# Performance work log

Hardware: AMD Instinct MI355X
Metric: run time of the kernel (lower is better)

The kernel has to match this reference:

```python
import jax, jax.numpy as jnp
import numpy as np

B, S, H, N, NREL = 16, 2048, 1024, 128, 8


def setup_inputs() -> dict:
    key = jax.random.key(0)
    ks = jax.random.split(key, 8)
    word_emb = jax.random.normal(ks[0], (B, S, H), dtype=jnp.float32)
    num_ids = jax.random.randint(ks[1], (B, N), 0, S)  # all valid (no -1 padding)
    is_response = jax.random.randint(ks[2], (B, N), 0, 2).astype(jnp.int32)
    numbers = jax.random.normal(ks[3], (B, N), dtype=jnp.float32)
    scale = 1.0 / np.sqrt(H).astype(np.float32)
    w_alpha = jax.random.normal(ks[4], (H, 1), dtype=jnp.float32) * scale
    b_alpha = jnp.zeros((1,), dtype=jnp.float32)
    w_f = jax.random.normal(ks[5], (H, H), dtype=jnp.float32) * scale
    b_f = jnp.zeros((H,), dtype=jnp.float32)
    W_r = jax.random.normal(ks[6], (NREL, H, H), dtype=jnp.float32) * scale  # 8 bias-free relation linears
    return dict(word_emb=word_emb, num_ids=num_ids, is_response=is_response,
                numbers=numbers, w_alpha=w_alpha, b_alpha=b_alpha,
                w_f=w_f, b_f=b_f, W_r=W_r)


def reference(word_emb, num_ids, is_response, numbers, w_alpha, b_alpha, w_f, b_f, W_r):
    Bn, Sn, Hn = word_emb.shape
    Nn = num_ids.shape[1]
    mask = (num_ids >= 0)  # [B,N] valid-node mask (original uses -1 padding)
    idx = jnp.clip(num_ids, 0, Sn - 1)
    # per-batch gather: Init[b,n] = word_emb[b, num_ids[b,n]]  -> [B,N,H]
    Init = jnp.take_along_axis(word_emb, idx[:, :, None], axis=1)
    alpha = jax.nn.sigmoid(Init @ w_alpha + b_alpha)  # [B,N,1]
    # all 8 relation transforms of every sender node j: T[b,r,j,:] = Init[b,j] @ W_r[r].T
    T = jnp.einsum('bnh,rkh->brnk', Init, W_r)  # [B,8,N,H]
    # relation id r(b,i,j) = 4*(num_i>num_j) + 2*resp_i + resp_j
    gt = (numbers[:, :, None] > numbers[:, None, :]).astype(jnp.int32)  # [B,N,N]
    resp = (is_response == 1).astype(jnp.int32)
    R = 4 * gt + 2 * resp[:, :, None] + resp[:, None, :]  # [B,N,N]
    sel = jax.nn.one_hot(R, NREL, dtype=word_emb.dtype)  # [B,N,N,8]
    not_diag = ~jnp.eye(Nn, dtype=bool)
    # edge weight over sender j: alpha_j, valid i & j, i != j
    wgt = (alpha[:, None, :, 0] * mask[:, None, :] * mask[:, :, None]
           * not_diag[None]).astype(word_emb.dtype)  # [B,N,N]
    Temp = jnp.einsum('bijr,brjh->bih', sel * wgt[..., None], T)  # [B,N,H]
    n_nodes = mask.sum(axis=1)  # [B]
    denom = jnp.maximum(n_nodes - 1, 1).astype(word_emb.dtype)
    Temp = Temp / denom[:, None, None]
    out = jax.nn.relu(Init @ w_f + b_f + Temp)  # [B,N,H]
    return out
```

## Files before the change

kernel.cpp:

```cpp
#include <hip/hip_runtime.h>
#include <hip/hip_bf16.h>
#include <stdint.h>

#define B_ 16
#define S_ 2048
#define H_ 1024
#define N_ 128
#define M_ (B_*N_)
#define K5 5120
#define MP 2176

typedef __attribute__((ext_vector_type(8))) short s8vec;
typedef __attribute__((ext_vector_type(4))) short s4vec;
typedef __attribute__((ext_vector_type(4))) float f4vec;
typedef __hip_bfloat16 bf16;

__global__ void k_sortmeta(const int* __restrict__ num_ids, const int* __restrict__ is_resp,
                           const float* __restrict__ numbers,
                           int* __restrict__ sigma, int* __restrict__ newgrp,
                           int* __restrict__ respv, float* __restrict__ denom,
                           int* __restrict__ aperm, int* __restrict__ iperm,
                           int* __restrict__ meta) {
    __shared__ float nums_s[2048];
    __shared__ int sig_s[2048];
    __shared__ int s0[1024], s1[1024];
    __shared__ int cnt_s[16];
    int t = threadIdx.x;
    int g0 = 2*t, g1 = 2*t + 1;
    int b = g0 >> 7;
    int i0 = g0 & 127, i1 = g1 & 127;
    float n0 = numbers[g0], n1 = numbers[g1];
    int id0 = num_ids[g0], id1 = num_ids[g1];
    int v0 = (id0 >= 0) ? 1 : 0, v1 = (id1 >= 0) ? 1 : 0;
    int rsp0 = (is_resp[g0] == 1) ? 1 : 0, rsp1 = (is_resp[g1] == 1) ? 1 : 0;
    nums_s[g0] = n0; nums_s[g1] = n1;
    if (t < 16) cnt_s[t] = 0;
    aperm[t] = -1; aperm[t + 1024] = -1;
    if (t < MP - 2048) aperm[t + 2048] = -1;
    __syncthreads();
    const float* nb = nums_s + b*N_;
    int p0 = 0, p1 = 0;
    for (int j = 0; j < N_; ++j) {
        float nj = nb[j];
        p0 += (nj < n0 || (nj == n0 && j < i0)) ? 1 : 0;
        p1 += (nj < n1 || (nj == n1 && j < i1)) ? 1 : 0;
    }
    sig_s[b*N_ + p0] = i0;
    sig_s[b*N_ + p1] = i1;
    atomicAdd(&cnt_s[b], v0 + v1);
    __syncthreads();
    sigma[g0] = sig_s[g0]; sigma[g1] = sig_s[g1];
    {
        int cur = sig_s[g0];
        int prv = (i0 > 0) ? sig_s[g0-1] : 0;
        newgrp[g0] = (i0 == 0 || nb[cur] != nb[prv]) ? 1 : 0;
        cur = sig_s[g1];
        prv = sig_s[g1-1];
        newgrp[g1] = (nb[cur] != nb[prv]) ? 1 : 0;
    }
    respv[g0] = rsp0 | (v0 << 1);
    respv[g1] = rsp1 | (v1 << 1);
    if (t < 16) denom[t] = fmaxf((float)(cnt_s[t] - 1), 1.0f);
    int a0 = 1 - rsp0, b0 = 1 - rsp1;
    s0[t] = a0 + b0;
    s1[t] = rsp0 + rsp1;
    __syncthreads();
    for (int off = 1; off < 1024; off <<= 1) {
        int w0 = (t >= off) ? s0[t-off] : 0;
        int w1 = (t >= off) ? s1[t-off] : 0;
        __syncthreads();
        s0[t] += w0; s1[t] += w1;
        __syncthreads();
    }
    int C0 = s0[1023], C1 = s1[1023];
    int P0 = ((C0 + 127) >> 7) << 7;
    int ex0 = s0[t] - (a0 + b0);
    int ex1 = s1[t] - (rsp0 + rsp1);
    int p_a = (rsp0 == 0) ? ex0 : P0 + ex1;
    int p_b = (rsp1 == 0) ? ex0 + a0 : P0 + ex1 + rsp0;
    aperm[p_a] = g0; iperm[g0] = p_a;
    aperm[p_b] = g1; iperm[g1] = p_b;
    if (t == 0) { meta[0] = P0; meta[1] = C0; meta[2] = C1; }
}

__global__ void k_prep(const float* __restrict__ word_emb, const int* __restrict__ num_ids,
                       const float* __restrict__ w_alpha, const float* __restrict__ b_alpha,
                       const float* __restrict__ denom, const int* __restrict__ iperm,
                       const float* __restrict__ W_r, const float* __restrict__ w_f,
                       bf16* __restrict__ A, float* __restrict__ ascaled,
                       bf16* __restrict__ Wt) {
    __shared__ float lds[64][65];
    int bid = blockIdx.x;
    int t = threadIdx.x;
    if (bid < 2048) {
        int b = bid >> 7, n = bid & 127;
        int idv = num_ids[b*N_ + n];
        int valid = (idv >= 0) ? 1 : 0;
        int idx = idv < 0 ? 0 : (idv > S_-1 ? S_-1 : idv);
        int pr = iperm[b*N_ + n];
        const float4* row = (const float4*)(word_emb + ((size_t)b*S_ + idx)*H_);
        float4 v = row[t];
        float4 w = ((const float4*)w_alpha)[t];
        float part = v.x*w.x + v.y*w.y + v.z*w.z + v.w*w.w;
        union { s4vec v4; bf16 h[4]; } pk;
        pk.h[0] = __float2bfloat16(v.x);
        pk.h[1] = __float2bfloat16(v.y);
        pk.h[2] = __float2bfloat16(v.z);
        pk.h[3] = __float2bfloat16(v.w);
        *(s4vec*)(A + (size_t)pr*K5 + 4*H_ + t*4) = pk.v4;
#pragma unroll
        for (int off = 32; off > 0; off >>= 1) part += __shfl_down(part, off, 64);
        if ((t & 63) == 0) lds[0][t >> 6] = part;
        __syncthreads();
        if (t == 0) {
            float dot = lds[0][0] + lds[0][1] + lds[0][2] + lds[0][3] + b_alpha[0];
            float al = 1.0f / (1.0f + __expf(-dot));
            ascaled[b*N_ + n] = valid ? (al / denom[b]) : 0.0f;
        }
        return;
    }
    if (bid < 6144) {
        size_t o = ((size_t)(bid - 2048)*256 + t)*8;
        int cs = (int)(o >> 20);
        int c = cs >> 2, s = cs & 3;
        int r = ((s >> 1) << 2) + 2*c + (s & 1);
        size_t off = o & (size_t)(H_*H_ - 1);
        const float4* src = (const float4*)(W_r + (size_t)r*H_*H_ + off);
        float4 v0 = src[0], v1 = src[1];
        union { s8vec v8; bf16 h[8]; } pk;
        pk.h[0] = __float2bfloat16(v0.x); pk.h[1] = __float2bfloat16(v0.y);
        pk.h[2] = __float2bfloat16(v0.z); pk.h[3] = __float2bfloat16(v0.w);
        pk.h[4] = __float2bfloat16(v1.x); pk.h[5] = __float2bfloat16(v1.y);
        pk.h[6] = __float2bfloat16(v1.z); pk.h[7] = __float2bfloat16(v1.w);
        *(s8vec*)(Wt + (size_t)(c*5 + s)*H_*H_ + off) = pk.v8;
        return;
    }
    int bb = bid - 6144;
    int bi = bb & 15, bj = bb >> 4;
    int ty = t >> 4, tx = t & 15;
#pragma unroll
    for (int i = 0; i < 4; ++i) {
        int r = ty*4 + i;
        float4 v = *(const float4*)(w_f + (size_t)(bi*64 + r)*H_ + bj*64 + tx*4);
        lds[r][tx*4+0] = v.x; lds[r][tx*4+1] = v.y;
        lds[r][tx*4+2] = v.z; lds[r][tx*4+3] = v.w;
    }
    __syncthreads();
    bf16* d0 = Wt + (size_t)4*H_*H_;
    bf16* d1 = Wt + (size_t)9*H_*H_;
#pragma unroll
    for (int i = 0; i < 4; ++i) {
        int n = ty*4 + i;
        size_t doff = (size_t)(bj*64 + n)*H_ + bi*64 + tx*4;
        union { s4vec v4; bf16 h[4]; } pk;
#pragma unroll
        for (int j = 0; j < 4; ++j) pk.h[j] = __float2bfloat16(lds[tx*4+j][n]);
        *(s4vec*)(d0 + doff) = pk.v4;
        *(s4vec*)(d1 + doff) = pk.v4;
    }
}

__global__ void k_build(const float* __restrict__ ascaled, const int* __restrict__ sigma,
                        const int* __restrict__ newgrp, const int* __restrict__ respv,
                        const int* __restrict__ iperm, bf16* __restrict__ A) {
    int b = blockIdx.y;
    int h = blockIdx.x*64 + threadIdx.x;
    __shared__ float as_s[N_];
    __shared__ int sig_s[N_], ng_s[N_], rv_s[N_], pm_s[N_];
    for (int j = threadIdx.x; j < N_; j += 64) {
        as_s[j] = ascaled[b*N_ + j];
        sig_s[j] = sigma[b*N_ + j];
        ng_s[j] = newgrp[b*N_ + j];
        rv_s[j] = respv[b*N_ + j];
        pm_s[j] = iperm[b*N_ + j];
    }
    __syncthreads();
    const bf16* initcol = A + 4*H_ + h;
    float tot0 = 0.f, tot1 = 0.f;
#pragma unroll 8
    for (int i2 = 0; i2 < N_; ++i2) {
        float v = as_s[i2] * __bfloat162float(initcol[(size_t)pm_s[i2]*K5]);
        if (rv_s[i2] & 1) tot1 += v; else tot0 += v;
    }
    float cS0=0.f, cS1=0.f, cG0=0.f, cG1=0.f;
#pragma unroll 8
    for (int p = 0; p < N_; ++p) {
        int i2 = sig_s[p];
        if (ng_s[p]) { cS0 += cG0; cS1 += cG1; cG0 = 0.f; cG1 = 0.f; }
        float v = as_s[i2] * __bfloat162float(initcol[(size_t)pm_s[i2]*K5]);
        int resp = rv_s[i2] & 1;
        float vf = (rv_s[i2] >> 1) ? 1.0f : 0.0f;
        float G0 = cS0, G1 = cS1;
        float L0 = tot0 - G0 - (resp ? 0.f : v);
        float L1 = tot1 - G1 - (resp ? v : 0.f);
        bf16* Ar = A + (size_t)pm_s[i2]*K5 + h;
        Ar[0*H_] = __float2bfloat16(L0*vf);
        Ar[1*H_] = __float2bfloat16(L1*vf);
        Ar[2*H_] = __float2bfloat16(G0*vf);
        Ar[3*H_] = __float2bfloat16(G1*vf);
        if (resp) cG1 += v; else cG0 += v;
    }
}

#define BM 64
#define BN 64
#define BK 64
#define NSTEP (K5/BK)

__global__ __launch_bounds__(256, 2) void k_gemm(const bf16* __restrict__ A,
                                                 const bf16* __restrict__ Wt,
                                                 const int* __restrict__ meta,
                                                 const int* __restrict__ aperm,
                                                 const float* __restrict__ b_f,
                                                 float* __restrict__ out) {
    __shared__ __align__(16) bf16 As0[BM*BK], As1[BM*BK], As2[BM*BK], As3[BM*BK];
    __shared__ __align__(16) bf16 Bs0[BN*BK], Bs1[BN*BK], Bs2[BN*BK], Bs3[BN*BK];
    int tid = threadIdx.x;
    int w = tid >> 6, lane = tid & 63;
    int q = lane >> 4, r = lane & 15;
    int bid = blockIdx.x;
    int wg = (bid & 7)*68 + (bid >> 3);
    int mt = wg % 34, nt = wg / 34;
    int rowBase = mt * BM, colBase = nt * BN;
    int wm = w >> 1, wn = w & 1;
    int P0 = meta[0];
    const bf16* Wtc = Wt + ((rowBase >= P0) ? (size_t)5*H_*H_ : 0);

    int og[2][4];
    float bias[2];
#pragma unroll
    for (int mi = 0; mi < 2; ++mi) {
        int rb = rowBase + wm*32 + mi*16 + q*4;
#pragma unroll
        for (int e = 0; e < 4; ++e) og[mi][e] = aperm[rb + e];
    }
#pragma unroll
    for (int ni = 0; ni < 2; ++ni) bias[ni] = b_f[colBase + wn*32 + ni*16 + r];
#pragma unroll
    for (int mi = 0; mi < 2; ++mi)
#pragma unroll
        for (int e = 0; e < 4; ++e) asm volatile("" : "+v"(og[mi][e]));
    asm volatile("" : "+v"(bias[0]), "+v"(bias[1]));
    asm volatile("s_waitcnt vmcnt(0)" ::: "memory");

    f4vec acc[2][2];
#pragma unroll
    for (int mi = 0; mi < 2; ++mi)
#pragma unroll
        for (int ni = 0; ni < 2; ++ni)
#pragma unroll
            for (int e = 0; e < 4; ++e) acc[mi][ni][e] = 0.0f;

    auto STAGE = [&](bf16* AsB, bf16* BsB, int kin) {
        int slot = kin >> 10, koff = kin & 1023;
        const bf16* Wslot = Wtc + ((size_t)slot << 20);
#pragma unroll
        for (int j = 0; j < 2; ++j) {
            int c = tid + j*256;
            int row = c >> 3;
            int p = (c & 7) ^ (row & 7);
            const bf16* ga = A + (size_t)(rowBase + row)*K5 + kin + p*8;
            __builtin_amdgcn_global_load_lds((const __attribute__((address_space(1))) void*)ga,
                (__attribute__((address_space(3))) void*)((char*)AsB + j*4096 + w*1024), 16, 0, 0);
            const bf16* gb = Wslot + ((size_t)(colBase + row) << 10) + koff + p*8;
            __builtin_amdgcn_global_load_lds((const __attribute__((address_space(1))) void*)gb,
                (__attribute__((address_space(3))) void*)((char*)BsB + j*4096 + w*1024), 16, 0, 0);
        }
    };

    auto COMPUTE = [&](const bf16* AsB, const bf16* BsB) {
        const short* Asp = (const short*)AsB;
        const short* Bsp = (const short*)BsB;
        s8vec af[2][2], bfr[2][2];
#pragma unroll
        for (int kk = 0; kk < 2; ++kk) {
            int sl = ((kk*4 + q) ^ (r & 7)) << 3;
#pragma unroll
            for (int mi = 0; mi < 2; ++mi)
                af[kk][mi] = *(const s8vec*)(Asp + (wm*32 + mi*16 + r)*BK + sl);
#pragma unroll
            for (int ni = 0; ni < 2; ++ni)
                bfr[kk][ni] = *(const s8vec*)(Bsp + (wn*32 + ni*16 + r)*BK + sl);
        }
#pragma unroll
        for (int kk = 0; kk < 2; ++kk)
#pragma unroll
            for (int mi = 0; mi < 2; ++mi)
#pragma unroll
                for (int ni = 0; ni < 2; ++ni)
                    acc[mi][ni] = __builtin_amdgcn_mfma_f32_16x16x32_bf16(
                        af[kk][mi], bfr[kk][ni], acc[mi][ni], 0, 0, 0);
    };

#define SLOT8(CA, CB, SA, SB, tnext)                              \
    asm volatile("s_waitcnt vmcnt(8)" ::: "memory");              \
    __builtin_amdgcn_s_barrier();                                 \
    __builtin_amdgcn_sched_barrier(0);                            \
    STAGE(SA, SB, (tnext)*BK);                                    \
    COMPUTE(CA, CB);                                              \
    __builtin_amdgcn_sched_barrier(0);

    STAGE(As0, Bs0, 0);
    STAGE(As1, Bs1, BK);
    STAGE(As2, Bs2, 2*BK);

    for (int tt = 0; tt < NSTEP - 4; tt += 4) {
        SLOT8(As0, Bs0, As3, Bs3, tt + 3);
        SLOT8(As1, Bs1, As0, Bs0, tt + 4);
        SLOT8(As2, Bs2, As1, Bs1, tt + 5);
        SLOT8(As3, Bs3, As2, Bs2, tt + 6);
    }
    asm volatile("s_waitcnt vmcnt(8)" ::: "memory");
    __builtin_amdgcn_s_barrier();
    __builtin_amdgcn_sched_barrier(0);
    STAGE(As3, Bs3, 79*BK);
    COMPUTE(As0, Bs0);
    __builtin_amdgcn_sched_barrier(0);
    asm volatile("s_waitcnt vmcnt(8)" ::: "memory");
    __builtin_amdgcn_s_barrier();
    __builtin_amdgcn_sched_barrier(0);
    COMPUTE(As1, Bs1);
    __builtin_amdgcn_sched_barrier(0);
    asm volatile("s_waitcnt vmcnt(4)" ::: "memory");
    __builtin_amdgcn_s_barrier();
    __builtin_amdgcn_sched_barrier(0);
    COMPUTE(As2, Bs2);
    __builtin_amdgcn_sched_barrier(0);
    asm volatile("s_waitcnt vmcnt(0)" ::: "memory");
    __builtin_amdgcn_s_barrier();
    __builtin_amdgcn_sched_barrier(0);
    COMPUTE(As3, Bs3);
#undef SLOT8

#pragma unroll
    for (int mi = 0; mi < 2; ++mi) {
#pragma unroll
        for (int ni = 0; ni < 2; ++ni) {
            int cc = colBase + wn*32 + ni*16 + r;
            if (og[mi][0] >= 0) out[(size_t)og[mi][0]*H_ + cc] = fmaxf(acc[mi][ni][0] + bias[ni], 0.0f);
            if (og[mi][1] >= 0) out[(size_t)og[mi][1]*H_ + cc] = fmaxf(acc[mi][ni][1] + bias[ni], 0.0f);
            if (og[mi][2] >= 0) out[(size_t)og[mi][2]*H_ + cc] = fmaxf(acc[mi][ni][2] + bias[ni], 0.0f);
            if (og[mi][3] >= 0) out[(size_t)og[mi][3]*H_ + cc] = fmaxf(acc[mi][ni][3] + bias[ni], 0.0f);
        }
    }
}

extern "C" void kernel_launch(void* const* d_in, const int* in_sizes, int n_in,
                              void* d_out, int out_size, void* d_ws, size_t ws_size,
                              hipStream_t stream) {
    (void)in_sizes; (void)n_in; (void)out_size; (void)ws_size;
    const float* word_emb = (const float*)d_in[0];
    const int*   num_ids  = (const int*)d_in[1];
    const int*   is_resp  = (const int*)d_in[2];
    const float* numbers  = (const float*)d_in[3];
    const float* w_alpha  = (const float*)d_in[4];
    const float* b_alpha  = (const float*)d_in[5];
    const float* w_f      = (const float*)d_in[6];
    const float* b_f      = (const float*)d_in[7];
    const float* W_r      = (const float*)d_in[8];
    float* out = (float*)d_out;

    char* ws = (char*)d_ws;
    bf16*  Aws     = (bf16*)(ws);
    bf16*  Wt      = (bf16*)(ws + 22282240);
    float* ascaled = (float*)(ws + 52166656);
    int*   sigma   = (int*)(ws + 52174848);
    int*   newgrp  = (int*)(ws + 52183040);
    int*   respv   = (int*)(ws + 52191232);
    float* denom   = (float*)(ws + 52199424);
    int*   aperm   = (int*)(ws + 52199488);
    int*   iperm   = (int*)(ws + 52208192);
    int*   meta    = (int*)(ws + 52216384);

    k_sortmeta<<<1, 1024, 0, stream>>>(num_ids, is_resp, numbers, sigma, newgrp, respv,
                                       denom, aperm, iperm, meta);
    k_prep  <<<6400, 256, 0, stream>>>(word_emb, num_ids, w_alpha, b_alpha, denom, iperm,
                                       W_r, w_f, Aws, ascaled, Wt);
    k_build <<<dim3(16,16), 64, 0, stream>>>(ascaled, sigma, newgrp, respv, iperm, Aws);
    k_gemm  <<<544,  256, 0, stream>>>(Aws, Wt, meta, aperm, b_f, out);
}
```

Before: 309.3 us.

## Enlarge GEMM tiles to 128x128 with split-K and a separate reduction epilogue

The GEMM output tile grows from 64x64 to 128x128, each wave now owning a 64x64 sub-tile, to raise data reuse per LDS load. K is split four ways so the grid keeps its 544 blocks. Each block writes fp32 partial sums to a workspace buffer, and a new epilogue kernel sums the four partials, adds the bias, applies ReLU and un-permutes rows. The 4-stage LDS pipeline becomes a double buffer with full vmcnt(0) waits, which exposes more load latency. The partial-sum buffer also adds roughly 35 MB of extra global write and read traffic.

```diff
diff --git a/kernel.cpp b/kernel.cpp
--- a/kernel.cpp
+++ b/kernel.cpp
@@ -202,52 +202,38 @@
     }
 }
 
-#define BM 64
-#define BN 64
+#define BM 128
+#define BN 128
 #define BK 64
-#define NSTEP (K5/BK)
+#define KS 4
+#define KSP (K5/KS)
+#define NSTEP (KSP/BK)
 
 __global__ __launch_bounds__(256, 2) void k_gemm(const bf16* __restrict__ A,
                                                  const bf16* __restrict__ Wt,
                                                  const int* __restrict__ meta,
-                                                 const int* __restrict__ aperm,
-                                                 const float* __restrict__ b_f,
-                                                 float* __restrict__ out) {
-    __shared__ __align__(16) bf16 As0[BM*BK], As1[BM*BK], As2[BM*BK], As3[BM*BK];
-    __shared__ __align__(16) bf16 Bs0[BN*BK], Bs1[BN*BK], Bs2[BN*BK], Bs3[BN*BK];
+                                                 float* __restrict__ P) {
+    __shared__ __align__(16) bf16 As0[BM*BK], As1[BM*BK];
+    __shared__ __align__(16) bf16 Bs0[BN*BK], Bs1[BN*BK];
     int tid = threadIdx.x;
     int w = tid >> 6, lane = tid & 63;
     int q = lane >> 4, r = lane & 15;
     int bid = blockIdx.x;
     int wg = (bid & 7)*68 + (bid >> 3);
-    int mt = wg % 34, nt = wg / 34;
+    int mt = wg % 17;
+    int rest = wg / 17;
+    int nt = rest & 7, ks = rest >> 3;
     int rowBase = mt * BM, colBase = nt * BN;
     int wm = w >> 1, wn = w & 1;
     int P0 = meta[0];
     const bf16* Wtc = Wt + ((rowBase >= P0) ? (size_t)5*H_*H_ : 0);
-
-    int og[2][4];
-    float bias[2];
-#pragma unroll
-    for (int mi = 0; mi < 2; ++mi) {
-        int rb = rowBase + wm*32 + mi*16 + q*4;
-#pragma unroll
-        for (int e = 0; e < 4; ++e) og[mi][e] = aperm[rb + e];
-    }
-#pragma unroll
-    for (int ni = 0; ni < 2; ++ni) bias[ni] = b_f[colBase + wn*32 + ni*16 + r];
-#pragma unroll
-    for (int mi = 0; mi < 2; ++mi)
-#pragma unroll
-        for (int e = 0; e < 4; ++e) asm volatile("" : "+v"(og[mi][e]));
-    asm volatile("" : "+v"(bias[0]), "+v"(bias[1]));
-    asm volatile("s_waitcnt vmcnt(0)" ::: "memory");
-
-    f4vec acc[2][2];
-#pragma unroll
-    for (int mi = 0; mi < 2; ++mi)
-#pragma unroll
-        for (int ni = 0; ni < 2; ++ni)
+    const int kb = ks * KSP;
+
+    f4vec acc[4][4];
+#pragma unroll
+    for (int mi = 0; mi < 4; ++mi)
+#pragma unroll
+        for (int ni = 0; ni < 4; ++ni)
 #pragma unroll
             for (int e = 0; e < 4; ++e) acc[mi][ni][e] = 0.0f;
 
@@ -255,7 +241,7 @@
         int slot = kin >> 10, koff = kin & 1023;
         const bf16* Wslot = Wtc + ((size_t)slot << 20);
 #pragma unroll
-        for (int j = 0; j < 2; ++j) {
+        for (int j = 0; j < 4; ++j) {
             int c = tid + j*256;
             int row = c >> 3;
             int p = (c & 7) ^ (row & 7);
@@ -271,78 +257,76 @@
     auto COMPUTE = [&](const bf16* AsB, const bf16* BsB) {
         const short* Asp = (const short*)AsB;
         const short* Bsp = (const short*)BsB;
-        s8vec af[2][2], bfr[2][2];
+        s8vec af[2][4], bfr[2][4];
 #pragma unroll
         for (int kk = 0; kk < 2; ++kk) {
             int sl = ((kk*4 + q) ^ (r & 7)) << 3;
 #pragma unroll
-            for (int mi = 0; mi < 2; ++mi)
-                af[kk][mi] = *(const s8vec*)(Asp + (wm*32 + mi*16 + r)*BK + sl);
-#pragma unroll
-            for (int ni = 0; ni < 2; ++ni)
-                bfr[kk][ni] = *(const s8vec*)(Bsp + (wn*32 + ni*16 + r)*BK + sl);
+            for (int mi = 0; mi < 4; ++mi)
+                af[kk][mi] = *(const s8vec*)(Asp + (wm*64 + mi*16 + r)*BK + sl);
+#pragma unroll
+            for (int ni = 0; ni < 4; ++ni)
+                bfr[kk][ni] = *(const s8vec*)(Bsp + (wn*64 + ni*16 + r)*BK + sl);
         }
 #pragma unroll
         for (int kk = 0; kk < 2; ++kk)
 #pragma unroll
-            for (int mi = 0; mi < 2; ++mi)
-#pragma unroll
-                for (int ni = 0; ni < 2; ++ni)
+            for (int mi = 0; mi < 4; ++mi)
+#pragma unroll
+                for (int ni = 0; ni < 4; ++ni)
                     acc[mi][ni] = __builtin_amdgcn_mfma_f32_16x16x32_bf16(
                         af[kk][mi], bfr[kk][ni], acc[mi][ni], 0, 0, 0);
     };
 
-#define SLOT8(CA, CB, SA, SB, tnext)                              \
-    asm volatile("s_waitcnt vmcnt(8)" ::: "memory");              \
-    __builtin_amdgcn_s_barrier();                                 \
-    __builtin_amdgcn_sched_barrier(0);                            \
-    STAGE(SA, SB, (tnext)*BK);                                    \
-    COMPUTE(CA, CB);                                              \
-    __builtin_amdgcn_sched_barrier(0);
-
-    STAGE(As0, Bs0, 0);
-    STAGE(As1, Bs1, BK);
-    STAGE(As2, Bs2, 2*BK);
-
-    for (int tt = 0; tt < NSTEP - 4; tt += 4) {
-        SLOT8(As0, Bs0, As3, Bs3, tt + 3);
-        SLOT8(As1, Bs1, As0, Bs0, tt + 4);
-        SLOT8(As2, Bs2, As1, Bs1, tt + 5);
-        SLOT8(As3, Bs3, As2, Bs2, tt + 6);
-    }
-    asm volatile("s_waitcnt vmcnt(8)" ::: "memory");
-    __builtin_amdgcn_s_barrier();
-    __builtin_amdgcn_sched_barrier(0);
-    STAGE(As3, Bs3, 79*BK);
-    COMPUTE(As0, Bs0);
-    __builtin_amdgcn_sched_barrier(0);
-    asm volatile("s_waitcnt vmcnt(8)" ::: "memory");
-    __builtin_amdgcn_s_barrier();
-    __builtin_amdgcn_sched_barrier(0);
-    COMPUTE(As1, Bs1);
-    __builtin_amdgcn_sched_barrier(0);
-    asm volatile("s_waitcnt vmcnt(4)" ::: "memory");
-    __builtin_amdgcn_s_barrier();
-    __builtin_amdgcn_sched_barrier(0);
-    COMPUTE(As2, Bs2);
-    __builtin_amdgcn_sched_barrier(0);
+    STAGE(As0, Bs0, kb);
     asm volatile("s_waitcnt vmcnt(0)" ::: "memory");
     __builtin_amdgcn_s_barrier();
     __builtin_amdgcn_sched_barrier(0);
-    COMPUTE(As3, Bs3);
-#undef SLOT8
-
-#pragma unroll
-    for (int mi = 0; mi < 2; ++mi) {
-#pragma unroll
-        for (int ni = 0; ni < 2; ++ni) {
-            int cc = colBase + wn*32 + ni*16 + r;
-            if (og[mi][0] >= 0) out[(size_t)og[mi][0]*H_ + cc] = fmaxf(acc[mi][ni][0] + bias[ni], 0.0f);
-            if (og[mi][1] >= 0) out[(size_t)og[mi][1]*H_ + cc] = fmaxf(acc[mi][ni][1] + bias[ni], 0.0f);
-            if (og[mi][2] >= 0) out[(size_t)og[mi][2]*H_ + cc] = fmaxf(acc[mi][ni][2] + bias[ni], 0.0f);
-            if (og[mi][3] >= 0) out[(size_t)og[mi][3]*H_ + cc] = fmaxf(acc[mi][ni][3] + bias[ni], 0.0f);
+
+    for (int t = 0; t < NSTEP; t += 2) {
+        STAGE(As1, Bs1, kb + (t + 1)*BK);
+        COMPUTE(As0, Bs0);
+        asm volatile("s_waitcnt vmcnt(0)" ::: "memory");
+        __builtin_amdgcn_s_barrier();
+        __builtin_amdgcn_sched_barrier(0);
+        if (t + 2 < NSTEP) STAGE(As0, Bs0, kb + (t + 2)*BK);
+        COMPUTE(As1, Bs1);
+        asm volatile("s_waitcnt vmcnt(0)" ::: "memory");
+        __builtin_amdgcn_s_barrier();
+        __builtin_amdgcn_sched_barrier(0);
+    }
+
+    float* Pk = P + (size_t)ks*MP*H_;
+#pragma unroll
+    for (int mi = 0; mi < 4; ++mi) {
+#pragma unroll
+        for (int ni = 0; ni < 4; ++ni) {
+            int cc = colBase + wn*64 + ni*16 + r;
+#pragma unroll
+            for (int e = 0; e < 4; ++e) {
+                int rr = rowBase + wm*64 + mi*16 + q*4 + e;
+                Pk[(size_t)rr*H_ + cc] = acc[mi][ni][e];
+            }
         }
     }
+}
+
+__global__ void k_epi(const float* __restrict__ P, const int* __restrict__ iperm,
+                      const float* __restrict__ b_f, float* __restrict__ out) {
+    int row = blockIdx.x;
+    int pr = iperm[row];
+    int t = threadIdx.x;
+    float4 v0 = ((const float4*)(P + ((size_t)0*MP + pr)*H_))[t];
+    float4 v1 = ((const float4*)(P + ((size_t)1*MP + pr)*H_))[t];
+    float4 v2 = ((const float4*)(P + ((size_t)2*MP + pr)*H_))[t];
+    float4 v3 = ((const float4*)(P + ((size_t)3*MP + pr)*H_))[t];
+    float4 bv = ((const float4*)b_f)[t];
+    float4 o;
+    o.x = fmaxf(v0.x + v1.x + v2.x + v3.x + bv.x, 0.0f);
+    o.y = fmaxf(v0.y + v1.y + v2.y + v3.y + bv.y, 0.0f);
+    o.z = fmaxf(v0.z + v1.z + v2.z + v3.z + bv.z, 0.0f);
+    o.w = fmaxf(v0.w + v1.w + v2.w + v3.w + bv.w, 0.0f);
+    ((float4*)(out + (size_t)row*H_))[t] = o;
 }
 
 extern "C" void kernel_launch(void* const* d_in, const int* in_sizes, int n_in,
@@ -363,19 +347,21 @@
     char* ws = (char*)d_ws;
     bf16*  Aws     = (bf16*)(ws);
     bf16*  Wt      = (bf16*)(ws + 22282240);
-    float* ascaled = (float*)(ws + 52166656);
-    int*   sigma   = (int*)(ws + 52174848);
-    int*   newgrp  = (int*)(ws + 52183040);
-    int*   respv   = (int*)(ws + 52191232);
-    float* denom   = (float*)(ws + 52199424);
-    int*   aperm   = (int*)(ws + 52199488);
-    int*   iperm   = (int*)(ws + 52208192);
-    int*   meta    = (int*)(ws + 52216384);
+    float* Pbuf    = (float*)(ws + 43253760);
+    float* ascaled = (float*)(ws + 78905344);
+    int*   sigma   = (int*)(ws + 78913536);
+    int*   newgrp  = (int*)(ws + 78921728);
+    int*   respv   = (int*)(ws + 78929920);
+    float* denom   = (float*)(ws + 78938112);
+    int*   aperm   = (int*)(ws + 78938176);
+    int*   iperm   = (int*)(ws + 78946880);
+    int*   meta    = (int*)(ws + 78955072);
 
     k_sortmeta<<<1, 1024, 0, stream>>>(num_ids, is_resp, numbers, sigma, newgrp, respv,
                                        denom, aperm, iperm, meta);
     k_prep  <<<6400, 256, 0, stream>>>(word_emb, num_ids, w_alpha, b_alpha, denom, iperm,
                                        W_r, w_f, Aws, ascaled, Wt);
     k_build <<<dim3(16,16), 64, 0, stream>>>(ascaled, sigma, newgrp, respv, iperm, Aws);
-    k_gemm  <<<544,  256, 0, stream>>>(Aws, Wt, meta, aperm, b_f, out);
-}
+    k_gemm  <<<544,  256, 0, stream>>>(Aws, Wt, meta, Pbuf);
+    k_epi   <<<2048, 256, 0, stream>>>(Pbuf, iperm, b_f, out);
+}
```

New measurement: 299.6 us. -3.1%, faster.
